# Performance work log

Hardware: AMD Instinct MI355X
Metric: run time of the kernel (lower is better)

The kernel has to match this reference:

```python
import jax, jax.numpy as jnp
import numpy as np

DIST_THRESH = 2.5


def _level_losses(lvl_cls, lvl_reg, gt_boxes, gt_labels):
    # lvl_cls: [B, HW, nc], lvl_reg: [B, HW, 4], gt_boxes: [B, N, 4], gt_labels: [B, N]
    gt_xy = gt_boxes[..., :2]            # [B, N, 2]
    pred_xy = lvl_reg[..., :2]           # [B, HW, 2]
    # squared euclidean distances [B, N, HW] (cdist equivalent; min/argmin unaffected by sqrt)
    d2 = jnp.sum((gt_xy[:, :, None, :] - pred_xy[:, None, :, :]) ** 2, axis=-1)
    min_d2 = jnp.min(d2, axis=2)         # [B, N]
    matches = jnp.argmin(d2, axis=2)     # [B, N]
    valid = jnp.sqrt(min_d2) < DIST_THRESH  # [B, N] bool
    # gather matched predictions per gt
    g_cls = jnp.take_along_axis(lvl_cls, matches[..., None], axis=1)   # [B, N, nc]
    g_reg = jnp.take_along_axis(lvl_reg, matches[..., None], axis=1)   # [B, N, 4]
    # cross entropy (reduction='none'), summed over valid matches
    logp = jax.nn.log_softmax(g_cls, axis=-1)
    ce = -jnp.take_along_axis(logp, gt_labels[..., None], axis=-1)[..., 0]  # [B, N]
    l1 = jnp.abs(g_reg - gt_boxes).sum(axis=-1)                             # [B, N]
    w = valid.astype(lvl_cls.dtype)
    return (ce * w).sum(), (l1 * w).sum(), w.sum()


def setup_inputs() -> dict:
    key = jax.random.key(0)
    ks = jax.random.split(key, 8)
    B, N, nc = 16, 128, 80
    hws = [25600, 6400, 1600]
    inp = {}
    for i, hw in enumerate(hws):
        inp[f"pred_cls_{i}"] = jax.random.normal(ks[i], (B, hw, nc), dtype=jnp.float32)
        inp[f"pred_reg_{i}"] = jax.random.normal(ks[3 + i], (B, hw, 4), dtype=jnp.float32)
    inp["gt_boxes"] = jax.random.normal(ks[6], (B, N, 4), dtype=jnp.float32)
    inp["gt_labels"] = jax.random.randint(ks[7], (B, N), 0, nc)
    return inp


def reference(pred_cls_0, pred_cls_1, pred_cls_2,
              pred_reg_0, pred_reg_1, pred_reg_2,
              gt_boxes, gt_labels):
    cls_list = [pred_cls_0, pred_cls_1, pred_cls_2]
    reg_list = [pred_reg_0, pred_reg_1, pred_reg_2]
    cls_loss = jnp.zeros((), jnp.float32)
    reg_loss = jnp.zeros((), jnp.float32)
    num_pos = jnp.zeros((), jnp.float32)
    for lvl_cls, lvl_reg in zip(cls_list, reg_list):
        c, r, n = _level_losses(lvl_cls, lvl_reg, gt_boxes, gt_labels)
        cls_loss = cls_loss + c
        reg_loss = reg_loss + r
        num_pos = num_pos + n
    denom = jnp.maximum(num_pos, 1.0)
    return cls_loss / denom, reg_loss / denom, num_pos
```

## Files before the change

kernel.cpp:

```cpp
#include <hip/hip_runtime.h>
#include <cstdint>
#include <cstddef>

#define NTH 256
#define NGT 128
#define BATCH 16
#define NC 80
#define G 16
#define NCHUNK (NGT / G)
#define HW0 25600
#define HW1 6400
#define HW2 1600
#define SL0 4
#define MAXSL 4
#define NLOSS_BLK (3 * BATCH * NGT / 4)

#define PACK0_OFF 0
#define PACK1_OFF (PACK0_OFF + BATCH * HW0 * 8)
#define PACK2_OFF (PACK1_OFF + BATCH * HW1 * 8)
#define PART_OFF  (PACK2_OFF + BATCH * HW2 * 8)
#define PART_BYTES (3 * BATCH * NGT * MAXSL * 8)
#define PARTL_OFF (PART_OFF + PART_BYTES)
#define PARTL_BYTES (NLOSS_BLK * 3 * sizeof(float))
#define WS_NEEDED (PARTL_OFF + (size_t)PARTL_BYTES)

__device__ __forceinline__ unsigned long long umin64(unsigned long long a, unsigned long long b) {
    return a < b ? a : b;
}

__global__ __launch_bounds__(NTH) void pack_kernel(
    const float* __restrict__ reg0, const float* __restrict__ reg1, const float* __restrict__ reg2,
    float2* __restrict__ xy0, float2* __restrict__ xy1, float2* __restrict__ xy2)
{
    int r = blockIdx.x * NTH + threadIdx.x;
    const int N0 = BATCH * HW0, N1 = BATCH * HW1, N2 = BATCH * HW2;
    if (r < N0) {
        float4 v = reinterpret_cast<const float4*>(reg0)[r];
        xy0[r] = make_float2(v.x, v.y);
    } else if (r < N0 + N1) {
        int i = r - N0;
        float4 v = reinterpret_cast<const float4*>(reg1)[i];
        xy1[i] = make_float2(v.x, v.y);
    } else if (r < N0 + N1 + N2) {
        int i = r - N0 - N1;
        float4 v = reinterpret_cast<const float4*>(reg2)[i];
        xy2[i] = make_float2(v.x, v.y);
    }
}

#define EVAL(px, py, idx_) do {                                                   \
    _Pragma("unroll")                                                             \
    for (int g = 0; g < G; ++g) {                                                 \
        float dx = gx[g] - (px), dy = gy[g] - (py);                               \
        float d2 = dx * dx + dy * dy;                                             \
        unsigned long long key =                                                  \
            ((unsigned long long)__float_as_uint(d2) << 32) | (unsigned)(idx_);   \
        kmin[g] = umin64(kmin[g], key);                                           \
    } } while (0)

__global__ __launch_bounds__(NTH) void scan_kernel(
    const float2* __restrict__ xy0, const float2* __restrict__ xy1, const float2* __restrict__ xy2,
    int stride2,
    const float* __restrict__ gt_boxes,
    unsigned long long* __restrict__ part)
{
    int x = blockIdx.x;
    int lvl, b, slice, chunk, HW, nsl;
    const float2* src;
    if (x < BATCH * SL0 * NCHUNK) {
        lvl = 0; b = x / (SL0 * NCHUNK);
        int r = x % (SL0 * NCHUNK);
        slice = r / NCHUNK; chunk = r % NCHUNK;
        HW = HW0; nsl = SL0; src = xy0;
    } else if (x < BATCH * SL0 * NCHUNK + BATCH * NCHUNK) {
        int y = x - BATCH * SL0 * NCHUNK;
        lvl = 1; b = y / NCHUNK; chunk = y % NCHUNK; slice = 0;
        HW = HW1; nsl = 1; src = xy1;
    } else {
        int y = x - BATCH * SL0 * NCHUNK - BATCH * NCHUNK;
        lvl = 2; b = y / NCHUNK; chunk = y % NCHUNK; slice = 0;
        HW = HW2; nsl = 1; src = xy2;
    }

    const int seg = HW / nsl;
    const int e0 = slice * seg, e1 = e0 + seg;
    const int tid = threadIdx.x, wave = tid >> 6, lane = tid & 63;
    const int n0 = chunk * G;

    float gx[G], gy[G];
#pragma unroll
    for (int g = 0; g < G; ++g) {
        const float* gb = gt_boxes + (size_t)(b * NGT + n0 + g) * 4;
        gx[g] = gb[0]; gy[g] = gb[1];
    }

    unsigned long long kmin[G];
#pragma unroll
    for (int g = 0; g < G; ++g) kmin[g] = ~0ull;

    if (stride2 == 1) {
        const float4* b4 = reinterpret_cast<const float4*>(src + (size_t)b * HW);
        for (int i = e0 / 2 + tid; i < e1 / 2; i += NTH) {
            float4 p = b4[i];
            int i0 = 2 * i;
            EVAL(p.x, p.y, i0);
            EVAL(p.z, p.w, i0 + 1);
        }
    } else {
        const float2* base = src + (size_t)b * HW * 2;
        for (int i = e0 + tid; i < e1; i += NTH) {
            float2 p = base[(size_t)i * 2];
            EVAL(p.x, p.y, i);
        }
    }

#pragma unroll
    for (int g = 0; g < G; ++g) {
#pragma unroll
        for (int off = 32; off >= 1; off >>= 1) {
            unsigned long long o = __shfl_down(kmin[g], off, 64);
            kmin[g] = umin64(kmin[g], o);
        }
    }

    __shared__ unsigned long long smem[G][4];
    if (lane == 0) {
#pragma unroll
        for (int g = 0; g < G; ++g) smem[g][wave] = kmin[g];
    }
    __syncthreads();

    if (tid < G) {
        unsigned long long key = umin64(umin64(smem[tid][0], smem[tid][1]),
                                        umin64(smem[tid][2], smem[tid][3]));
        part[((size_t)(lvl * BATCH + b) * NGT + n0 + tid) * MAXSL + slice] = key;
    }
}

__global__ __launch_bounds__(NTH) void loss_kernel(
    const float* __restrict__ cls0, const float* __restrict__ cls1, const float* __restrict__ cls2,
    const float* __restrict__ reg0, const float* __restrict__ reg1, const float* __restrict__ reg2,
    const float* __restrict__ gt_boxes, const int* __restrict__ gt_labels,
    const unsigned long long* __restrict__ part, float* __restrict__ partl)
{
    const int wave = threadIdx.x >> 6;
    const int lane = threadIdx.x & 63;
    const int gid = blockIdx.x * 4 + wave;
    const int lvl = gid / (BATCH * NGT);
    const int r = gid % (BATCH * NGT);
    const int b = r / NGT, n = r % NGT;

    const float* cls; const float* reg; int HW, S;
    if (lvl == 0)      { cls = cls0; reg = reg0; HW = HW0; S = SL0; }
    else if (lvl == 1) { cls = cls1; reg = reg1; HW = HW1; S = 1; }
    else               { cls = cls2; reg = reg2; HW = HW2; S = 1; }

    const unsigned long long* p = part + (size_t)gid * MAXSL;
    unsigned long long key = p[0];
    for (int s = 1; s < S; ++s) key = umin64(key, p[s]);

    int match = (int)(unsigned)(key & 0xffffffffu);
    float d2min = __uint_as_float((unsigned)(key >> 32));
    bool valid = d2min < 6.25f;

    const int label = gt_labels[b * NGT + n];
    const float* c = cls + ((size_t)b * HW + match) * NC;

    float x1 = c[lane];
    float x2 = (lane < NC - 64) ? c[64 + lane] : -INFINITY;
    float mx = fmaxf(x1, x2);
#pragma unroll
    for (int off = 32; off >= 1; off >>= 1) mx = fmaxf(mx, __shfl_xor(mx, off, 64));
    float s = expf(x1 - mx) + ((lane < NC - 64) ? expf(x2 - mx) : 0.0f);
#pragma unroll
    for (int off = 32; off >= 1; off >>= 1) s += __shfl_xor(s, off, 64);

    __shared__ float ce_s[4], l1_s[4], w_s[4];
    if (lane == 0) {
        float ce = 0.0f, l1 = 0.0f, w = 0.0f;
        if (valid) {
            float xlab = c[label];
            ce = -(xlab - mx - logf(s));
            const float* gb = gt_boxes + (size_t)(b * NGT + n) * 4;
            const float* gr = reg + ((size_t)b * HW + match) * 4;
            l1 = fabsf(gr[0] - gb[0]) + fabsf(gr[1] - gb[1]) +
                 fabsf(gr[2] - gb[2]) + fabsf(gr[3] - gb[3]);
            w = 1.0f;
        }
        ce_s[wave] = ce; l1_s[wave] = l1; w_s[wave] = w;
    }
    __syncthreads();

    if (threadIdx.x == 0) {
        float* o = partl + (size_t)blockIdx.x * 3;
        o[0] = ce_s[0] + ce_s[1] + ce_s[2] + ce_s[3];
        o[1] = l1_s[0] + l1_s[1] + l1_s[2] + l1_s[3];
        o[2] = w_s[0] + w_s[1] + w_s[2] + w_s[3];
    }
}

__global__ __launch_bounds__(NTH) void finalize_kernel(
    const float* __restrict__ partl, float* __restrict__ out)
{
    const int tid = threadIdx.x, wave = tid >> 6, lane = tid & 63;
    float ce = 0.0f, l1 = 0.0f, w = 0.0f;
    for (int i = tid; i < NLOSS_BLK; i += NTH) {
        ce += partl[(size_t)i * 3 + 0];
        l1 += partl[(size_t)i * 3 + 1];
        w  += partl[(size_t)i * 3 + 2];
    }
#pragma unroll
    for (int off = 32; off >= 1; off >>= 1) {
        ce += __shfl_xor(ce, off, 64);
        l1 += __shfl_xor(l1, off, 64);
        w  += __shfl_xor(w,  off, 64);
    }
    __shared__ float sm[3][4];
    if (lane == 0) { sm[0][wave] = ce; sm[1][wave] = l1; sm[2][wave] = w; }
    __syncthreads();
    if (tid == 0) {
        float tce = sm[0][0] + sm[0][1] + sm[0][2] + sm[0][3];
        float tl1 = sm[1][0] + sm[1][1] + sm[1][2] + sm[1][3];
        float tw  = sm[2][0] + sm[2][1] + sm[2][2] + sm[2][3];
        float denom = fmaxf(tw, 1.0f);
        out[0] = tce / denom;
        out[1] = tl1 / denom;
        out[2] = tw;
    }
}

extern "C" void kernel_launch(void* const* d_in, const int* in_sizes, int n_in,
                              void* d_out, int out_size, void* d_ws, size_t ws_size,
                              hipStream_t stream) {
    const float* cls0 = nullptr; const float* cls1 = nullptr; const float* cls2 = nullptr;
    const float* reg0 = nullptr; const float* reg1 = nullptr; const float* reg2 = nullptr;
    const float* gt_boxes = nullptr; const int* gt_labels = nullptr;
    for (int i = 0; i < n_in; ++i) {
        switch (in_sizes[i]) {
            case BATCH * HW0 * NC: cls0 = (const float*)d_in[i]; break;
            case BATCH * HW1 * NC: cls1 = (const float*)d_in[i]; break;
            case BATCH * HW2 * NC: cls2 = (const float*)d_in[i]; break;
            case BATCH * HW0 * 4:  reg0 = (const float*)d_in[i]; break;
            case BATCH * HW1 * 4:  reg1 = (const float*)d_in[i]; break;
            case BATCH * HW2 * 4:  reg2 = (const float*)d_in[i]; break;
            case BATCH * NGT * 4:  gt_boxes = (const float*)d_in[i]; break;
            case BATCH * NGT:      gt_labels = (const int*)d_in[i]; break;
            default: break;
        }
    }

    char* ws = (char*)d_ws;
    const bool pack = (ws_size >= WS_NEEDED);
    unsigned long long* part;
    float* partl;
    const int scan_grid = BATCH * SL0 * NCHUNK + 2 * BATCH * NCHUNK;

    if (pack) {
        float2* xy0 = (float2*)(ws + PACK0_OFF);
        float2* xy1 = (float2*)(ws + PACK1_OFF);
        float2* xy2 = (float2*)(ws + PACK2_OFF);
        part  = (unsigned long long*)(ws + PART_OFF);
        partl = (float*)(ws + PARTL_OFF);
        const int rows = BATCH * (HW0 + HW1 + HW2);
        pack_kernel<<<(rows + NTH - 1) / NTH, NTH, 0, stream>>>(
            reg0, reg1, reg2, xy0, xy1, xy2);
        scan_kernel<<<scan_grid, NTH, 0, stream>>>(
            xy0, xy1, xy2, 1, gt_boxes, part);
    } else {
        part  = (unsigned long long*)(ws);
        partl = (float*)(ws + PART_BYTES);
        scan_kernel<<<scan_grid, NTH, 0, stream>>>(
            (const float2*)reg0, (const float2*)reg1, (const float2*)reg2, 2,
            gt_boxes, part);
    }

    loss_kernel<<<NLOSS_BLK, NTH, 0, stream>>>(
        cls0, cls1, cls2, reg0, reg1, reg2, gt_boxes, gt_labels, part, partl);

    finalize_kernel<<<1, NTH, 0, stream>>>(partl, (float*)d_out);
}
```

Before: 220.8 us.

## Drop xy pack kernel and fold finalize into loss kernel via last-block counter

Removes the pack pass that copied xy coordinates into a compact buffer. The scan kernel now reads the full float4 regression rows directly, one point per thread per iteration. The separate finalize launch is replaced by an atomic counter: the last loss block to finish sums the partials and writes the output, and the counter is reset inside the scan kernel. This saves a kernel launch and the pack traffic, but the scan reads twice the bytes per point and evaluates one point per iteration instead of two.

After: 248.0 us. +12.3%, slower.

```diff
diff --git a/kernel.cpp b/kernel.cpp
--- a/kernel.cpp
+++ b/kernel.cpp
@@ -15,37 +15,14 @@
 #define MAXSL 4
 #define NLOSS_BLK (3 * BATCH * NGT / 4)
 
-#define PACK0_OFF 0
-#define PACK1_OFF (PACK0_OFF + BATCH * HW0 * 8)
-#define PACK2_OFF (PACK1_OFF + BATCH * HW1 * 8)
-#define PART_OFF  (PACK2_OFF + BATCH * HW2 * 8)
+#define PART_OFF   0
 #define PART_BYTES (3 * BATCH * NGT * MAXSL * 8)
-#define PARTL_OFF (PART_OFF + PART_BYTES)
-#define PARTL_BYTES (NLOSS_BLK * 3 * sizeof(float))
-#define WS_NEEDED (PARTL_OFF + (size_t)PARTL_BYTES)
+#define PARTL_OFF  PART_BYTES
+#define PARTL_BYTES (NLOSS_BLK * 3 * (int)sizeof(float))
+#define CNT_OFF    (PARTL_OFF + PARTL_BYTES)
 
 __device__ __forceinline__ unsigned long long umin64(unsigned long long a, unsigned long long b) {
     return a < b ? a : b;
-}
-
-__global__ __launch_bounds__(NTH) void pack_kernel(
-    const float* __restrict__ reg0, const float* __restrict__ reg1, const float* __restrict__ reg2,
-    float2* __restrict__ xy0, float2* __restrict__ xy1, float2* __restrict__ xy2)
-{
-    int r = blockIdx.x * NTH + threadIdx.x;
-    const int N0 = BATCH * HW0, N1 = BATCH * HW1, N2 = BATCH * HW2;
-    if (r < N0) {
-        float4 v = reinterpret_cast<const float4*>(reg0)[r];
-        xy0[r] = make_float2(v.x, v.y);
-    } else if (r < N0 + N1) {
-        int i = r - N0;
-        float4 v = reinterpret_cast<const float4*>(reg1)[i];
-        xy1[i] = make_float2(v.x, v.y);
-    } else if (r < N0 + N1 + N2) {
-        int i = r - N0 - N1;
-        float4 v = reinterpret_cast<const float4*>(reg2)[i];
-        xy2[i] = make_float2(v.x, v.y);
-    }
 }
 
 #define EVAL(px, py, idx_) do {                                                   \
@@ -59,27 +36,28 @@
     } } while (0)
 
 __global__ __launch_bounds__(NTH) void scan_kernel(
-    const float2* __restrict__ xy0, const float2* __restrict__ xy1, const float2* __restrict__ xy2,
-    int stride2,
+    const float4* __restrict__ reg0, const float4* __restrict__ reg1, const float4* __restrict__ reg2,
     const float* __restrict__ gt_boxes,
-    unsigned long long* __restrict__ part)
+    unsigned long long* __restrict__ part, unsigned int* __restrict__ counter)
 {
+    if (blockIdx.x == 0 && threadIdx.x == 0) *counter = 0u;
+
     int x = blockIdx.x;
     int lvl, b, slice, chunk, HW, nsl;
-    const float2* src;
+    const float4* src;
     if (x < BATCH * SL0 * NCHUNK) {
         lvl = 0; b = x / (SL0 * NCHUNK);
         int r = x % (SL0 * NCHUNK);
         slice = r / NCHUNK; chunk = r % NCHUNK;
-        HW = HW0; nsl = SL0; src = xy0;
+        HW = HW0; nsl = SL0; src = reg0;
     } else if (x < BATCH * SL0 * NCHUNK + BATCH * NCHUNK) {
         int y = x - BATCH * SL0 * NCHUNK;
         lvl = 1; b = y / NCHUNK; chunk = y % NCHUNK; slice = 0;
-        HW = HW1; nsl = 1; src = xy1;
+        HW = HW1; nsl = 1; src = reg1;
     } else {
         int y = x - BATCH * SL0 * NCHUNK - BATCH * NCHUNK;
         lvl = 2; b = y / NCHUNK; chunk = y % NCHUNK; slice = 0;
-        HW = HW2; nsl = 1; src = xy2;
+        HW = HW2; nsl = 1; src = reg2;
     }
 
     const int seg = HW / nsl;
@@ -98,20 +76,10 @@
 #pragma unroll
     for (int g = 0; g < G; ++g) kmin[g] = ~0ull;
 
-    if (stride2 == 1) {
-        const float4* b4 = reinterpret_cast<const float4*>(src + (size_t)b * HW);
-        for (int i = e0 / 2 + tid; i < e1 / 2; i += NTH) {
-            float4 p = b4[i];
-            int i0 = 2 * i;
-            EVAL(p.x, p.y, i0);
-            EVAL(p.z, p.w, i0 + 1);
-        }
-    } else {
-        const float2* base = src + (size_t)b * HW * 2;
-        for (int i = e0 + tid; i < e1; i += NTH) {
-            float2 p = base[(size_t)i * 2];
-            EVAL(p.x, p.y, i);
-        }
+    const float4* base = src + (size_t)b * HW;
+    for (int i = e0 + tid; i < e1; i += NTH) {
+        float4 p = base[i];
+        EVAL(p.x, p.y, i);
     }
 
 #pragma unroll
@@ -141,7 +109,8 @@
     const float* __restrict__ cls0, const float* __restrict__ cls1, const float* __restrict__ cls2,
     const float* __restrict__ reg0, const float* __restrict__ reg1, const float* __restrict__ reg2,
     const float* __restrict__ gt_boxes, const int* __restrict__ gt_labels,
-    const unsigned long long* __restrict__ part, float* __restrict__ partl)
+    const unsigned long long* __restrict__ part, float* __restrict__ partl,
+    unsigned int* __restrict__ counter, float* __restrict__ out)
 {
     const int wave = threadIdx.x >> 6;
     const int lane = threadIdx.x & 63;
@@ -176,6 +145,7 @@
     for (int off = 32; off >= 1; off >>= 1) s += __shfl_xor(s, off, 64);
 
     __shared__ float ce_s[4], l1_s[4], w_s[4];
+    __shared__ int is_last;
     if (lane == 0) {
         float ce = 0.0f, l1 = 0.0f, w = 0.0f;
         if (valid) {
@@ -196,36 +166,39 @@
         o[0] = ce_s[0] + ce_s[1] + ce_s[2] + ce_s[3];
         o[1] = l1_s[0] + l1_s[1] + l1_s[2] + l1_s[3];
         o[2] = w_s[0] + w_s[1] + w_s[2] + w_s[3];
-    }
-}
-
-__global__ __launch_bounds__(NTH) void finalize_kernel(
-    const float* __restrict__ partl, float* __restrict__ out)
-{
-    const int tid = threadIdx.x, wave = tid >> 6, lane = tid & 63;
-    float ce = 0.0f, l1 = 0.0f, w = 0.0f;
-    for (int i = tid; i < NLOSS_BLK; i += NTH) {
-        ce += partl[(size_t)i * 3 + 0];
-        l1 += partl[(size_t)i * 3 + 1];
-        w  += partl[(size_t)i * 3 + 2];
-    }
-#pragma unroll
-    for (int off = 32; off >= 1; off >>= 1) {
-        ce += __shfl_xor(ce, off, 64);
-        l1 += __shfl_xor(l1, off, 64);
-        w  += __shfl_xor(w,  off, 64);
-    }
-    __shared__ float sm[3][4];
-    if (lane == 0) { sm[0][wave] = ce; sm[1][wave] = l1; sm[2][wave] = w; }
+        __threadfence();
+        unsigned int old = atomicAdd(counter, 1u);
+        is_last = (old == (unsigned)(NLOSS_BLK - 1));
+    }
     __syncthreads();
-    if (tid == 0) {
-        float tce = sm[0][0] + sm[0][1] + sm[0][2] + sm[0][3];
-        float tl1 = sm[1][0] + sm[1][1] + sm[1][2] + sm[1][3];
-        float tw  = sm[2][0] + sm[2][1] + sm[2][2] + sm[2][3];
-        float denom = fmaxf(tw, 1.0f);
-        out[0] = tce / denom;
-        out[1] = tl1 / denom;
-        out[2] = tw;
+
+    if (is_last) {
+        __threadfence();
+        const int tid = threadIdx.x;
+        float ce = 0.0f, l1 = 0.0f, w = 0.0f;
+        for (int i = tid; i < NLOSS_BLK; i += NTH) {
+            ce += partl[(size_t)i * 3 + 0];
+            l1 += partl[(size_t)i * 3 + 1];
+            w  += partl[(size_t)i * 3 + 2];
+        }
+#pragma unroll
+        for (int off = 32; off >= 1; off >>= 1) {
+            ce += __shfl_xor(ce, off, 64);
+            l1 += __shfl_xor(l1, off, 64);
+            w  += __shfl_xor(w,  off, 64);
+        }
+        __shared__ float sm[3][4];
+        if (lane == 0) { sm[0][wave] = ce; sm[1][wave] = l1; sm[2][wave] = w; }
+        __syncthreads();
+        if (tid == 0) {
+            float tce = sm[0][0] + sm[0][1] + sm[0][2] + sm[0][3];
+            float tl1 = sm[1][0] + sm[1][1] + sm[1][2] + sm[1][3];
+            float tw  = sm[2][0] + sm[2][1] + sm[2][2] + sm[2][3];
+            float denom = fmaxf(tw, 1.0f);
+            out[0] = tce / denom;
+            out[1] = tl1 / denom;
+            out[2] = tw;
+        }
     }
 }
 
@@ -250,32 +223,16 @@
     }
 
     char* ws = (char*)d_ws;
-    const bool pack = (ws_size >= WS_NEEDED);
-    unsigned long long* part;
-    float* partl;
+    unsigned long long* part = (unsigned long long*)(ws + PART_OFF);
+    float* partl = (float*)(ws + PARTL_OFF);
+    unsigned int* counter = (unsigned int*)(ws + CNT_OFF);
+
     const int scan_grid = BATCH * SL0 * NCHUNK + 2 * BATCH * NCHUNK;
-
-    if (pack) {
-        float2* xy0 = (float2*)(ws + PACK0_OFF);
-        float2* xy1 = (float2*)(ws + PACK1_OFF);
-        float2* xy2 = (float2*)(ws + PACK2_OFF);
-        part  = (unsigned long long*)(ws + PART_OFF);
-        partl = (float*)(ws + PARTL_OFF);
-        const int rows = BATCH * (HW0 + HW1 + HW2);
-        pack_kernel<<<(rows + NTH - 1) / NTH, NTH, 0, stream>>>(
-            reg0, reg1, reg2, xy0, xy1, xy2);
-        scan_kernel<<<scan_grid, NTH, 0, stream>>>(
-            xy0, xy1, xy2, 1, gt_boxes, part);
-    } else {
-        part  = (unsigned long long*)(ws);
-        partl = (float*)(ws + PART_BYTES);
-        scan_kernel<<<scan_grid, NTH, 0, stream>>>(
-            (const float2*)reg0, (const float2*)reg1, (const float2*)reg2, 2,
-            gt_boxes, part);
-    }
+    scan_kernel<<<scan_grid, NTH, 0, stream>>>(
+        (const float4*)reg0, (const float4*)reg1, (const float4*)reg2,
+        gt_boxes, part, counter);
 
     loss_kernel<<<NLOSS_BLK, NTH, 0, stream>>>(
-        cls0, cls1, cls2, reg0, reg1, reg2, gt_boxes, gt_labels, part, partl);
-
-    finalize_kernel<<<1, NTH, 0, stream>>>(partl, (float*)d_out);
-}
+        cls0, cls1, cls2, reg0, reg1, reg2, gt_boxes, gt_labels,
+        part, partl, counter, (float*)d_out);
+}
```
